# Kernel tuning notes

Hardware: AMD Instinct MI355X
Metric: run time of the kernel (lower is better)

The kernel has to match this reference:

```python
import jax, jax.numpy as jnp
import numpy as np


def setup_inputs() -> dict:
    key = jax.random.key(0)
    ks = jax.random.split(key, 6)
    B, C, H, W, O = 8, 64, 64, 64, 64
    x = jax.random.normal(ks[0], (B, C, H, W), jnp.float32)
    wq = jax.random.normal(ks[1], (O, C), jnp.float32) * 0.1
    wk = jax.random.normal(ks[2], (O, C), jnp.float32) * 0.1
    wv = jax.random.normal(ks[3], (O, C), jnp.float32) * 0.1
    rel_w = jax.random.normal(ks[4], (O, W), jnp.float32)
    rel_h = jax.random.normal(ks[5], (O, H), jnp.float32)
    return {"x": x, "wq": wq, "wk": wk, "wv": wv,
            "rel_w": rel_w, "rel_h": rel_h,
            "kernel_size": 7, "padding": 3}


def reference(x, wq, wk, wv, rel_w, rel_h, kernel_size, padding):
    B, C, H, W = x.shape
    k, p = kernel_size, padding
    # 1x1 convs (no bias) == channel matmuls
    q = jnp.einsum('bchw,oc->bohw', x, wq)                      # [B,O,H,W]
    xp = jnp.pad(x, ((0, 0), (0, 0), (p, p), (p, p)))
    k_out = jnp.einsum('bchw,oc->bohw', xp, wk)                 # [B,O,H+2p,W+2p]
    v_out = jnp.einsum('bchw,oc->bohw', xp, wv)

    def patches(t):  # torch unfold(2).unfold(3) order: row offset slowest
        return jnp.stack([t[:, :, i:i + H, j:j + W]
                          for i in range(k) for j in range(k)], axis=-1)  # [B,O,H,W,k*k]

    kp = patches(k_out)
    vp = patches(v_out)
    # relative position logits (broadcast elementwise einsums)
    rel = q * rel_w[None, :, None, :] + q * rel_h[None, :, :, None]  # [B,O,H,W]
    logits = q[..., None] * kp + rel[..., None]                 # [B,O,H,W,k*k]
    attn = jax.nn.softmax(logits, axis=-1)
    return jnp.sum(attn * vp, axis=-1)                          # [B,O,H,W]
```

## Files before the change

### kernel.cpp

```cpp
#include <hip/hip_runtime.h>

#define HW 4096

__device__ float g_qkv[3 * 8 * 64 * HW];

#if __has_builtin(__builtin_amdgcn_exp2f)
#define QSCALE 1.4426950408889634f
__device__ __forceinline__ float fexp(float l) { return __builtin_amdgcn_exp2f(l); }
#else
#define QSCALE 1.0f
__device__ __forceinline__ float fexp(float l) { return __expf(l); }
#endif

__global__ __launch_bounds__(256, 2) void qkv_proj(
    const float* __restrict__ x,
    const float* __restrict__ wq,
    const float* __restrict__ wk,
    const float* __restrict__ wv)
{
    __shared__ float xs[64][64];
    __shared__ float wl[3][64][65];
    const int t = threadIdx.x;
    const int b = blockIdx.x >> 6;
    const int h = blockIdx.x & 63;

    {
        const float* __restrict__ mats[3] = { wq, wk, wv };
        #pragma unroll
        for (int m = 0; m < 3; ++m)
            for (int i = t; i < 4096; i += 256) {
                int o = i >> 6, c = i & 63;
                wl[m][o][c] = mats[m][i];
            }
        const float* xrow = x + (size_t)b * 64 * HW + (size_t)h * 64;
        for (int i = t; i < 4096; i += 256) {
            int c = i >> 6, w = i & 63;
            xs[c][w] = xrow[(size_t)c * HW + w];
        }
    }
    __syncthreads();

    const int w0 = (t & 15) * 4;
    const int o0 = (t >> 4) * 4;
    float acc[3][16];
    #pragma unroll
    for (int m = 0; m < 3; ++m)
        #pragma unroll
        for (int i = 0; i < 16; ++i) acc[m][i] = 0.f;

    #pragma unroll 4
    for (int cq = 0; cq < 16; ++cq) {
        const int c0 = cq * 4;
        float xa[4][4];
        #pragma unroll
        for (int ci = 0; ci < 4; ++ci)
            *(float4*)&xa[ci][0] = *(const float4*)&xs[c0 + ci][w0];
        #pragma unroll
        for (int m = 0; m < 3; ++m)
            #pragma unroll
            for (int oi = 0; oi < 4; ++oi) {
                #pragma unroll
                for (int ci = 0; ci < 4; ++ci) {
                    const float wv1 = wl[m][o0 + oi][c0 + ci];
                    #pragma unroll
                    for (int wi = 0; wi < 4; ++wi)
                        acc[m][oi * 4 + wi] = fmaf(wv1, xa[ci][wi], acc[m][oi * 4 + wi]);
                }
            }
    }

    #pragma unroll
    for (int m = 0; m < 3; ++m) {
        float* op = g_qkv + ((size_t)m * 8 + b) * (64 * HW) + (size_t)h * 64 + w0;
        #pragma unroll
        for (int oi = 0; oi < 4; ++oi) {
            float4 v = { acc[m][oi * 4 + 0], acc[m][oi * 4 + 1],
                         acc[m][oi * 4 + 2], acc[m][oi * 4 + 3] };
            *(float4*)&op[(size_t)(o0 + oi) * HW] = v;
        }
    }
}

__global__ __launch_bounds__(256, 2) void attn(float* __restrict__ out)
{
    __shared__ float kv[70][140];
    const int t = threadIdx.x;
    const int b = blockIdx.x >> 6;
    const int o = blockIdx.x & 63;

    const float* qb = g_qkv + ((size_t)(0 * 8 + b) * 64 + o) * HW;
    const float* kb = g_qkv + ((size_t)(1 * 8 + b) * 64 + o) * HW;
    const float* vb = g_qkv + ((size_t)(2 * 8 + b) * 64 + o) * HW;

    for (int i = t; i < 70 * 70; i += 256) {
        int r = i / 70, c = i - r * 70;
        int gh = r - 3, gw = c - 3;
        float kk = 0.f, vv = 0.f;
        if ((unsigned)gh < 64u && (unsigned)gw < 64u) {
            kk = kb[gh * 64 + gw];
            vv = vb[gh * 64 + gw];
        }
        kv[r][c] = kk;
        kv[r][70 + c] = vv;
    }
    __syncthreads();

    const int r0 = (t >> 4) * 4;
    const int c0 = (t & 15) * 4;

    float qv[16], den[16], num[16];
    #pragma unroll
    for (int i = 0; i < 4; ++i) {
        float4 q4 = *(const float4*)&qb[(r0 + i) * 64 + c0];
        qv[i * 4 + 0] = q4.x * QSCALE; qv[i * 4 + 1] = q4.y * QSCALE;
        qv[i * 4 + 2] = q4.z * QSCALE; qv[i * 4 + 3] = q4.w * QSCALE;
    }
    #pragma unroll
    for (int i = 0; i < 16; ++i) { den[i] = 0.f; num[i] = 0.f; }

    #pragma unroll
    for (int rr = 0; rr < 10; ++rr) {
        #pragma unroll
        for (int cc = 0; cc < 10; ++cc) {
            const float kk = kv[r0 + rr][c0 + cc];
            const float vv = kv[r0 + rr][70 + c0 + cc];
            #pragma unroll
            for (int i = 0; i < 4; ++i) {
                if (rr - i >= 0 && rr - i < 7) {
                    #pragma unroll
                    for (int j = 0; j < 4; ++j) {
                        if (cc - j >= 0 && cc - j < 7) {
                            float e = fexp(qv[i * 4 + j] * kk);
                            den[i * 4 + j] += e;
                            num[i * 4 + j] = fmaf(e, vv, num[i * 4 + j]);
                        }
                    }
                }
            }
        }
    }

    float* ob = out + ((size_t)(b * 64 + o)) * HW;
    #pragma unroll
    for (int i = 0; i < 4; ++i) {
        float4 v = { num[i * 4 + 0] / den[i * 4 + 0], num[i * 4 + 1] / den[i * 4 + 1],
                     num[i * 4 + 2] / den[i * 4 + 2], num[i * 4 + 3] / den[i * 4 + 3] };
        *(float4*)&ob[(r0 + i) * 64 + c0] = v;
    }
}

extern "C" void kernel_launch(void* const* d_in, const int* in_sizes, int n_in,
                              void* d_out, int out_size, void* d_ws, size_t ws_size,
                              hipStream_t stream)
{
    qkv_proj<<<dim3(512), dim3(256), 0, stream>>>(
        (const float*)d_in[0], (const float*)d_in[1],
        (const float*)d_in[2], (const float*)d_in[3]);
    attn<<<dim3(512), dim3(256), 0, stream>>>((float*)d_out);
}
```

Measured before the change: 116.7 us.

## Use packed float2 math in projection and attention kernels, retile projection

Both kernels are rewritten to use two-wide float vectors so the compiler can emit packed FP32 instructions (v_pk_fma/v_pk_mul/v_pk_add) for the channel matmul and the attention multiply/accumulate. The projection thread tile changes from 4 outputs x 4 columns to 2 outputs x 8 columns to fit the paired layout. The attention kernel's launch bound is raised to 3 blocks per SIMD to encourage higher occupancy. Exp still runs per lane, and tighter register limits could cause spills.

```diff
diff --git a/kernel.cpp b/kernel.cpp
--- a/kernel.cpp
+++ b/kernel.cpp
@@ -1,6 +1,8 @@
 #include <hip/hip_runtime.h>
 
 #define HW 4096
+
+typedef float v2f __attribute__((ext_vector_type(2)));
 
 __device__ float g_qkv[3 * 8 * 64 * HW];
 
@@ -40,48 +42,56 @@
     }
     __syncthreads();
 
-    const int w0 = (t & 15) * 4;
-    const int o0 = (t >> 4) * 4;
-    float acc[3][16];
+    const int w0 = (t & 7) * 8;
+    const int o0 = (t >> 3) * 2;
+
+    v2f acc[3][2][4];
     #pragma unroll
     for (int m = 0; m < 3; ++m)
         #pragma unroll
-        for (int i = 0; i < 16; ++i) acc[m][i] = 0.f;
+        for (int oi = 0; oi < 2; ++oi)
+            #pragma unroll
+            for (int wp = 0; wp < 4; ++wp) acc[m][oi][wp] = (v2f){0.f, 0.f};
 
     #pragma unroll 4
     for (int cq = 0; cq < 16; ++cq) {
         const int c0 = cq * 4;
-        float xa[4][4];
+        v2f xa[4][4];
         #pragma unroll
-        for (int ci = 0; ci < 4; ++ci)
-            *(float4*)&xa[ci][0] = *(const float4*)&xs[c0 + ci][w0];
+        for (int ci = 0; ci < 4; ++ci) {
+            float4 a = *(const float4*)&xs[c0 + ci][w0];
+            float4 c = *(const float4*)&xs[c0 + ci][w0 + 4];
+            xa[ci][0] = (v2f){a.x, a.y}; xa[ci][1] = (v2f){a.z, a.w};
+            xa[ci][2] = (v2f){c.x, c.y}; xa[ci][3] = (v2f){c.z, c.w};
+        }
         #pragma unroll
         for (int m = 0; m < 3; ++m)
             #pragma unroll
-            for (int oi = 0; oi < 4; ++oi) {
+            for (int oi = 0; oi < 2; ++oi)
                 #pragma unroll
                 for (int ci = 0; ci < 4; ++ci) {
                     const float wv1 = wl[m][o0 + oi][c0 + ci];
+                    const v2f ws = (v2f){wv1, wv1};
                     #pragma unroll
-                    for (int wi = 0; wi < 4; ++wi)
-                        acc[m][oi * 4 + wi] = fmaf(wv1, xa[ci][wi], acc[m][oi * 4 + wi]);
+                    for (int wp = 0; wp < 4; ++wp)
+                        acc[m][oi][wp] += ws * xa[ci][wp];
                 }
-            }
     }
 
     #pragma unroll
     for (int m = 0; m < 3; ++m) {
         float* op = g_qkv + ((size_t)m * 8 + b) * (64 * HW) + (size_t)h * 64 + w0;
         #pragma unroll
-        for (int oi = 0; oi < 4; ++oi) {
-            float4 v = { acc[m][oi * 4 + 0], acc[m][oi * 4 + 1],
-                         acc[m][oi * 4 + 2], acc[m][oi * 4 + 3] };
-            *(float4*)&op[(size_t)(o0 + oi) * HW] = v;
+        for (int oi = 0; oi < 2; ++oi) {
+            float4 v0 = { acc[m][oi][0].x, acc[m][oi][0].y, acc[m][oi][1].x, acc[m][oi][1].y };
+            float4 v1 = { acc[m][oi][2].x, acc[m][oi][2].y, acc[m][oi][3].x, acc[m][oi][3].y };
+            *(float4*)&op[(size_t)(o0 + oi) * HW]     = v0;
+            *(float4*)&op[(size_t)(o0 + oi) * HW + 4] = v1;
         }
     }
 }
 
-__global__ __launch_bounds__(256, 2) void attn(float* __restrict__ out)
+__global__ __launch_bounds__(256, 3) void attn(float* __restrict__ out)
 {
     __shared__ float kv[70][140];
     const int t = threadIdx.x;
@@ -108,15 +118,15 @@
     const int r0 = (t >> 4) * 4;
     const int c0 = (t & 15) * 4;
 
-    float qv[16], den[16], num[16];
+    v2f qv2[4][2], den2[4][2], num2[4][2];
     #pragma unroll
     for (int i = 0; i < 4; ++i) {
         float4 q4 = *(const float4*)&qb[(r0 + i) * 64 + c0];
-        qv[i * 4 + 0] = q4.x * QSCALE; qv[i * 4 + 1] = q4.y * QSCALE;
-        qv[i * 4 + 2] = q4.z * QSCALE; qv[i * 4 + 3] = q4.w * QSCALE;
+        qv2[i][0] = (v2f){q4.x * QSCALE, q4.y * QSCALE};
+        qv2[i][1] = (v2f){q4.z * QSCALE, q4.w * QSCALE};
+        den2[i][0] = (v2f){0.f, 0.f}; den2[i][1] = (v2f){0.f, 0.f};
+        num2[i][0] = (v2f){0.f, 0.f}; num2[i][1] = (v2f){0.f, 0.f};
     }
-    #pragma unroll
-    for (int i = 0; i < 16; ++i) { den[i] = 0.f; num[i] = 0.f; }
 
     #pragma unroll
     for (int rr = 0; rr < 10; ++rr) {
@@ -124,15 +134,29 @@
         for (int cc = 0; cc < 10; ++cc) {
             const float kk = kv[r0 + rr][c0 + cc];
             const float vv = kv[r0 + rr][70 + c0 + cc];
+            const v2f ks = (v2f){kk, kk};
+            const v2f vs = (v2f){vv, vv};
             #pragma unroll
             for (int i = 0; i < 4; ++i) {
                 if (rr - i >= 0 && rr - i < 7) {
                     #pragma unroll
-                    for (int j = 0; j < 4; ++j) {
-                        if (cc - j >= 0 && cc - j < 7) {
-                            float e = fexp(qv[i * 4 + j] * kk);
-                            den[i * 4 + j] += e;
-                            num[i * 4 + j] = fmaf(e, vv, num[i * 4 + j]);
+                    for (int jp = 0; jp < 2; ++jp) {
+                        const int j0 = 2 * jp, j1 = 2 * jp + 1;
+                        const bool a0 = (cc - j0 >= 0) && (cc - j0 < 7);
+                        const bool a1 = (cc - j1 >= 0) && (cc - j1 < 7);
+                        if (a0 && a1) {
+                            v2f l = qv2[i][jp] * ks;
+                            v2f e = (v2f){fexp(l.x), fexp(l.y)};
+                            den2[i][jp] += e;
+                            num2[i][jp] += e * vs;
+                        } else if (a0) {
+                            float e = fexp(qv2[i][jp].x * kk);
+                            den2[i][jp].x += e;
+                            num2[i][jp].x = fmaf(e, vv, num2[i][jp].x);
+                        } else if (a1) {
+                            float e = fexp(qv2[i][jp].y * kk);
+                            den2[i][jp].y += e;
+                            num2[i][jp].y = fmaf(e, vv, num2[i][jp].y);
                         }
                     }
                 }
@@ -143,8 +167,8 @@
     float* ob = out + ((size_t)(b * 64 + o)) * HW;
     #pragma unroll
     for (int i = 0; i < 4; ++i) {
-        float4 v = { num[i * 4 + 0] / den[i * 4 + 0], num[i * 4 + 1] / den[i * 4 + 1],
-                     num[i * 4 + 2] / den[i * 4 + 2], num[i * 4 + 3] / den[i * 4 + 3] };
+        float4 v = { num2[i][0].x / den2[i][0].x, num2[i][0].y / den2[i][0].y,
+                     num2[i][1].x / den2[i][1].x, num2[i][1].y / den2[i][1].y };
         *(float4*)&ob[(r0 + i) * 64 + c0] = v;
     }
 }
```

Result: slower. 232.8 us (+99.4%).
